# Performance work log

Hardware: AMD Instinct MI355X
Metric: run time of the kernel (lower is better)

Reference implementation:

```python
import jax, jax.numpy as jnp
import numpy as np

B, N, DIM, H, DH = 2, 2048, 1024, 16, 64
INNER = H * DH
EPS = 1e-12  # F.normalize eps
MAX_LOG_SCALE = np.log(1.0 / 0.01)  # clamp max for logit_scale


def setup_inputs() -> dict:
    key = jax.random.key(0)
    k1, k2, k3, k4 = jax.random.split(key, 4)
    x = jax.random.normal(k1, (B, N, DIM), dtype=jnp.float32)
    # Linear weights stored as [in, out] (transpose of torch's [out, in])
    w_qkv = jax.random.normal(k2, (DIM, 3 * INNER), dtype=jnp.float32) * (DIM ** -0.5)
    w_out = jax.random.normal(k3, (INNER, DIM), dtype=jnp.float32) * (INNER ** -0.5)
    b_out = jax.random.normal(k4, (DIM,), dtype=jnp.float32) * 0.01
    logit_scale = jnp.full((H, 1, 1), jnp.log(10.0), dtype=jnp.float32)
    return {"x": x, "w_qkv": w_qkv, "w_out": w_out, "b_out": b_out,
            "logit_scale": logit_scale}


def reference(x, w_qkv, w_out, b_out, logit_scale):
    b, n, dim = x.shape
    h = logit_scale.shape[0]
    qkv = x @ w_qkv                              # [b, n, 3*inner]
    q, k, v = jnp.split(qkv, 3, axis=-1)
    split_heads = lambda t: t.reshape(b, n, h, -1).transpose(0, 2, 1, 3)  # b h n d
    q, k, v = split_heads(q), split_heads(k), split_heads(v)
    # L2-normalize q and k (F.normalize semantics: divide by max(norm, eps))
    qn = q / jnp.maximum(jnp.linalg.norm(q, axis=-1, keepdims=True), EPS)
    kn = k / jnp.maximum(jnp.linalg.norm(k, axis=-1, keepdims=True), EPS)
    scale = jnp.exp(jnp.minimum(logit_scale, MAX_LOG_SCALE))  # [h,1,1], per-head temp
    cos_dots = jnp.einsum('bhid,bhjd->bhij', qn, kn) * scale   # [b,h,n,n]
    # NOTE: masking in the source mutates the unused plain-dot `dots` tensor,
    # so the output never depends on the mask -> faithfully omitted.
    attn = jax.nn.softmax(cos_dots, axis=-1)
    out = jnp.einsum('bhij,bhjd->bhid', attn, v)               # [b,h,n,d]
    out = out.transpose(0, 2, 1, 3).reshape(b, n, -1)          # [b,n,inner]
    return out @ w_out + b_out
```

## Files before the change

### kernel.cpp

```cpp
#include <hip/hip_runtime.h>

typedef __attribute__((ext_vector_type(8))) short bf16x8;
typedef __attribute__((ext_vector_type(4))) float f32x4;
typedef __attribute__((ext_vector_type(16))) float f32x16;
typedef unsigned short u16;
typedef unsigned int u32;
typedef __attribute__((ext_vector_type(4))) unsigned int u32x4;

#define DEV static __device__ __forceinline__

DEV u16 f2bf(float f) {
  u32 u = __float_as_uint(f);
  u += 0x7FFFu + ((u >> 16) & 1u);
  return (u16)(u >> 16);
}
DEV float bf2f(u16 h) { return __uint_as_float(((u32)h) << 16); }

DEV void gload16(const void* g, void* l) {
  __builtin_amdgcn_global_load_lds((const __attribute__((address_space(1))) void*)g,
                                   (__attribute__((address_space(3))) void*)l, 16, 0, 0);
}

#define MFMA16(a, b, c) __builtin_amdgcn_mfma_f32_16x16x32_bf16((a), (b), (c), 0, 0, 0)
#define MFMA32(a, b, c) __builtin_amdgcn_mfma_f32_32x32x16_bf16((a), (b), (c), 0, 0, 0)

DEV u32 cvtpk(float lo, float hi) {
  u32 r;
  asm("v_cvt_pk_bf16_f32 %0, %1, %2" : "=v"(r) : "v"(lo), "v"(hi));
  return r;
}
DEV void plswap(u32& a, u32& b) {
  asm volatile("v_permlane32_swap_b32 %0, %1" : "+v"(a), "+v"(b));
}
DEV bf16x8 asbf(u32x4 v) {
  union { u32x4 u; bf16x8 b; } x;
  x.u = v;
  return x.b;
}

DEV void rawbar() {
  __builtin_amdgcn_sched_barrier(0);
  asm volatile("" ::: "memory");
  __builtin_amdgcn_s_barrier();
  asm volatile("" ::: "memory");
  __builtin_amdgcn_sched_barrier(0);
}
#define VMCNT4() asm volatile("s_waitcnt vmcnt(4)" ::: "memory")
#define VMCNT0() asm volatile("s_waitcnt vmcnt(0)" ::: "memory")
#define LGKM0()  asm volatile("s_waitcnt lgkmcnt(0)" ::: "memory")

#define MAXLOG 4.6051701859880914f

__global__ __launch_bounds__(256) void k_prep(const float* __restrict__ x,
                                              u16* __restrict__ Xbf,
                                              const float* __restrict__ w_qkv,
                                              u16* __restrict__ Wqkvt,
                                              const float* __restrict__ w_out,
                                              u16* __restrict__ Woutt) {
  __shared__ u16 lds[64][72];
  int blk = blockIdx.x;
  int t = threadIdx.x;
  if (blk < 2048) {
    int i = blk * 256 + t;
    const f32x4* p = (const f32x4*)(x + (size_t)i * 8);
    f32x4 a = p[0], b = p[1];
    bf16x8 o;
    o[0] = (short)f2bf(a[0]); o[1] = (short)f2bf(a[1]);
    o[2] = (short)f2bf(a[2]); o[3] = (short)f2bf(a[3]);
    o[4] = (short)f2bf(b[0]); o[5] = (short)f2bf(b[1]);
    o[6] = (short)f2bf(b[2]); o[7] = (short)f2bf(b[3]);
    *(bf16x8*)(Xbf + (size_t)i * 8) = o;
    return;
  }
  const float* src;
  u16* dst;
  int rows, cols, bx, by;
  if (blk < 2816) {
    int q = blk - 2048;
    src = w_qkv; dst = Wqkvt; rows = 1024; cols = 3072;
    bx = q % 48; by = q / 48;
  } else {
    int q = blk - 2816;
    src = w_out; dst = Woutt; rows = 1024; cols = 1024;
    bx = q % 16; by = q / 16;
  }
  int r0 = by * 64, c0 = bx * 64;
  int r = t >> 2, cq = (t & 3) << 4;
  const float* s = src + (size_t)(r0 + r) * cols + c0 + cq;
#pragma unroll
  for (int i = 0; i < 16; i += 4) {
    f32x4 v = *(const f32x4*)(s + i);
    lds[r][cq + i + 0] = f2bf(v[0]);
    lds[r][cq + i + 1] = f2bf(v[1]);
    lds[r][cq + i + 2] = f2bf(v[2]);
    lds[r][cq + i + 3] = f2bf(v[3]);
  }
  __syncthreads();
  int c = t >> 2, rq = (t & 3) << 4;
  bf16x8 o0, o1;
#pragma unroll
  for (int i = 0; i < 8; ++i) o0[i] = (short)lds[rq + i][c];
#pragma unroll
  for (int i = 0; i < 8; ++i) o1[i] = (short)lds[rq + 8 + i][c];
  u16* d = dst + (size_t)(c0 + c) * rows + r0 + rq;
  *(bf16x8*)d = o0;
  *(bf16x8*)(d + 8) = o1;
}

__global__ __launch_bounds__(256) void k_gemm_qkv(const u16* __restrict__ A,
                                                  const u16* __restrict__ Bt,
                                                  const float* __restrict__ logit_scale,
                                                  u16* __restrict__ Qn, u16* __restrict__ Kn,
                                                  u16* __restrict__ Vt,
                                                  int M, int N, int K, int nbx) {
  __shared__ __align__(16) u16 lsA[128 * 64];
  __shared__ __align__(16) u16 lsB[128 * 64];
  int tid = threadIdx.x;
  int lane = tid & 63, wave = tid >> 6;
  int wr = (wave >> 1) * 64, wc = (wave & 1) * 64;
  int nwg = gridDim.x;
  int orig = blockIdx.x;
  int wg = (orig & 7) * (nwg >> 3) + (orig >> 3);
  int bm = (wg / nbx) * 128, bn = (wg % nbx) * 128;

  f32x4 acc[4][4] = {};

  const u16* aSrc[4];
  const u16* bSrc[4];
  int lOf[4];
#pragma unroll
  for (int i = 0; i < 4; ++i) {
    int c = i * 256 + tid;
    int row = c >> 3, ch = c & 7;
    int g = ch ^ (row & 7);
    aSrc[i] = A + (size_t)(bm + row) * K + g * 8;
    bSrc[i] = Bt + (size_t)(bn + row) * K + g * 8;
    lOf[i] = c * 8;
  }

  for (int k0 = 0; k0 < K; k0 += 64) {
    __syncthreads();
#pragma unroll
    for (int i = 0; i < 4; ++i) gload16(aSrc[i] + k0, &lsA[lOf[i]]);
#pragma unroll
    for (int i = 0; i < 4; ++i) gload16(bSrc[i] + k0, &lsB[lOf[i]]);
    __syncthreads();
#pragma unroll
    for (int kk = 0; kk < 2; ++kk) {
      bf16x8 af[4], bfr[4];
#pragma unroll
      for (int m = 0; m < 4; ++m) {
        int r = wr + m * 16 + (lane & 15);
        int p = (kk * 4 + (lane >> 4)) ^ (r & 7);
        af[m] = *(const bf16x8*)&lsA[r * 64 + p * 8];
      }
#pragma unroll
      for (int n = 0; n < 4; ++n) {
        int r = wc + n * 16 + (lane & 15);
        int p = (kk * 4 + (lane >> 4)) ^ (r & 7);
        bfr[n] = *(const bf16x8*)&lsB[r * 64 + p * 8];
      }
#pragma unroll
      for (int m = 0; m < 4; ++m)
#pragma unroll
        for (int n = 0; n < 4; ++n)
          acc[m][n] = MFMA16(af[m], bfr[n], acc[m][n]);
    }
  }

  int colg = bn + wc;
  if (colg < 2048) {
    bool isQ = colg < 1024;
    int h = (colg >> 6) & 15;
    float scale = isQ ? __expf(fminf(logit_scale[h], MAXLOG)) : 1.0f;
    u16* dst = isQ ? Qn : Kn;
#pragma unroll
    for (int m = 0; m < 4; ++m) {
#pragma unroll
      for (int j = 0; j < 4; ++j) {
        float ss = 0.f;
#pragma unroll
        for (int n = 0; n < 4; ++n) ss += acc[m][n][j] * acc[m][n][j];
        ss += __shfl_xor(ss, 1, 64);
        ss += __shfl_xor(ss, 2, 64);
        ss += __shfl_xor(ss, 4, 64);
        ss += __shfl_xor(ss, 8, 64);
        float r = scale / fmaxf(sqrtf(ss), 1e-12f);
        int row = bm + wr + m * 16 + ((lane >> 4) << 2) + j;
        int b = row >> 11, tok = row & 2047;
        size_t base = ((size_t)(b * 16 + h) * 2048 + tok) * 64;
#pragma unroll
        for (int n = 0; n < 4; ++n)
          dst[base + n * 16 + (lane & 15)] = f2bf(acc[m][n][j] * r);
      }
    }
  } else {
    int h = ((colg - 2048) >> 6) & 15;
    __syncthreads();
    u16* sl = (wave < 2 ? lsA : lsB) + (wave & 1) * 2048;
    int bb = bm >> 11, bmm = bm & 2047;
    size_t vbase = ((size_t)(bb * 16 + h) * 64) * 2048;
#pragma unroll
    for (int rr = 0; rr < 2; ++rr) {
#pragma unroll
      for (int nn = 0; nn < 2; ++nn) {
        int n = rr * 2 + nn;
        int d32 = nn * 16 + (lane & 15);
        int xr = (d32 & 7) << 3;
#pragma unroll
        for (int m = 0; m < 4; ++m)
#pragma unroll
          for (int j = 0; j < 4; ++j) {
            int tok = m * 16 + ((lane >> 4) << 2) + j;
            sl[d32 * 64 + (tok ^ xr)] = f2bf(acc[m][n][j]);
          }
      }
      LGKM0();
#pragma unroll
      for (int ri = 0; ri < 4; ++ri) {
        int li = ri * 64 + lane;
        int d32 = li >> 3, c = li & 7;
        int cx = c ^ (d32 & 7);
        bf16x8 v = *(const bf16x8*)&sl[d32 * 64 + cx * 8];
        size_t dsto = vbase + (size_t)(rr * 32 + d32) * 2048 + bmm + wr + c * 8;
        *(bf16x8*)&Vt[dsto] = v;
      }
      LGKM0();
    }
  }
}

__global__ __launch_bounds__(256) void k_gemm_out(const u16* __restrict__ A,
                                                  const u16* __restrict__ Bt,
                                                  float* __restrict__ Cout,
                                                  const float* __restrict__ bias,
                                                  int M, int N, int K, int nbx) {
  __shared__ __align__(16) u16 lsA[128 * 64];
  __shared__ __align__(16) u16 lsB[64 * 64];
  int tid = threadIdx.x;
  int lane = tid & 63, wave = tid >> 6;
  int wr = (wave >> 1) * 64, wc = (wave & 1) * 32;
  int nwg = gridDim.x;
  int orig = blockIdx.x;
  int wg = (orig & 7) * (nwg >> 3) + (orig >> 3);
  int bm = (wg / nbx) * 128, bn = (wg % nbx) * 64;

  f32x4 acc[4][2] = {};

  const u16* aSrc[4];
  const u16* bSrc[2];
  int lOfA[4], lOfB[2];
#pragma unroll
  for (int i = 0; i < 4; ++i) {
    int c = i * 256 + tid;
    int row = c >> 3, ch = c & 7;
    int g = ch ^ (row & 7);
    aSrc[i] = A + (size_t)(bm + row) * K + g * 8;
    lOfA[i] = c * 8;
  }
#pragma unroll
  for (int i = 0; i < 2; ++i) {
    int c = i * 256 + tid;
    int row = c >> 3, ch = c & 7;
    int g = ch ^ (row & 7);
    bSrc[i] = Bt + (size_t)(bn + row) * K + g * 8;
    lOfB[i] = c * 8;
  }

  for (int k0 = 0; k0 < K; k0 += 64) {
    __syncthreads();
#pragma unroll
    for (int i = 0; i < 4; ++i) gload16(aSrc[i] + k0, &lsA[lOfA[i]]);
#pragma unroll
    for (int i = 0; i < 2; ++i) gload16(bSrc[i] + k0, &lsB[lOfB[i]]);
    __syncthreads();
#pragma unroll
    for (int kk = 0; kk < 2; ++kk) {
      bf16x8 af[4], bfr[2];
#pragma unroll
      for (int m = 0; m < 4; ++m) {
        int r = wr + m * 16 + (lane & 15);
        int p = (kk * 4 + (lane >> 4)) ^ (r & 7);
        af[m] = *(const bf16x8*)&lsA[r * 64 + p * 8];
      }
#pragma unroll
      for (int n = 0; n < 2; ++n) {
        int r = wc + n * 16 + (lane & 15);
        int p = (kk * 4 + (lane >> 4)) ^ (r & 7);
        bfr[n] = *(const bf16x8*)&lsB[r * 64 + p * 8];
      }
#pragma unroll
      for (int m = 0; m < 4; ++m)
#pragma unroll
        for (int n = 0; n < 2; ++n)
          acc[m][n] = MFMA16(af[m], bfr[n], acc[m][n]);
    }
  }

#pragma unroll
  for (int m = 0; m < 4; ++m) {
    int row = bm + wr + m * 16 + ((lane >> 4) << 2);
#pragma unroll
    for (int n = 0; n < 2; ++n) {
      int col = bn + wc + n * 16 + (lane & 15);
      float bb = bias[col];
#pragma unroll
      for (int j = 0; j < 4; ++j)
        Cout[(size_t)(row + j) * N + col] = acc[m][n][j] + bb;
    }
  }
}

__global__ __launch_bounds__(256, 2) void k_flash(const u16* __restrict__ Qn,
                                                  const u16* __restrict__ Kn,
                                                  const u16* __restrict__ Vt,
                                                  const float* __restrict__ logit_scale,
                                                  u16* __restrict__ AO) {
  __shared__ __align__(16) u16 lsK[2][64 * 64];
  __shared__ __align__(16) u16 lsV[2][64 * 64];
  __shared__ float l_s[4][32];
  int tid = threadIdx.x, lane = tid & 63, wave = tid >> 6;
  int r31 = lane & 31, h = lane >> 5;
  int bh = blockIdx.x, b = bh >> 4, hd = bh & 15;
  int qw = blockIdx.y * 128 + wave * 32;
  const u16* Q = Qn + (size_t)bh * 2048 * 64;
  const u16* Kb = Kn + (size_t)bh * 2048 * 64;
  const u16* Vb = Vt + (size_t)bh * 64 * 2048;

  float negC = -__expf(fminf(logit_scale[hd], MAXLOG));

  bf16x8 qB[4];
#pragma unroll
  for (int ks = 0; ks < 4; ++ks)
    qB[ks] = *(const bf16x8*)&Q[(size_t)(qw + r31) * 64 + ks * 16 + h * 8];

  size_t kGO[2], vGO[2];
  int lOff[2];
#pragma unroll
  for (int j = 0; j < 2; ++j) {
    int s = j * 256 + tid;
    int row = s >> 3, ch = s & 7, g = ch ^ (row & 7);
    kGO[j] = (size_t)row * 64 + g * 8;
    vGO[j] = (size_t)row * 2048 + g * 8;
    lOff[j] = s * 8;
  }

  int off[2][4];
#pragma unroll
  for (int a = 0; a < 2; ++a)
#pragma unroll
    for (int ks = 0; ks < 4; ++ks)
      off[a][ks] = (a * 32 + r31) * 64 + ((((ks << 1) | h) ^ (r31 & 7)) << 3);

  f32x16 o0, o1;
#pragma unroll
  for (int i = 0; i < 16; ++i) { o0[i] = 0.f; o1[i] = 0.f; }
  float lsm[4] = {0.f, 0.f, 0.f, 0.f};

#define STAGE(dstbuf, kvt)                                          \
  {                                                                 \
    size_t kv0 = (size_t)(kvt) * 64;                                \
    gload16(Kb + kv0 * 64 + kGO[0], &lsK[dstbuf][lOff[0]]);         \
    gload16(Kb + kv0 * 64 + kGO[1], &lsK[dstbuf][lOff[1]]);         \
    gload16(Vb + kv0 + vGO[0], &lsV[dstbuf][lOff[0]]);              \
    gload16(Vb + kv0 + vGO[1], &lsV[dstbuf][lOff[1]]);              \
  }

  STAGE(0, 0);

#pragma unroll 1
  for (int t = 0; t < 32; ++t) {
    int cur = t & 1;
    if (t < 31) {
      STAGE(cur ^ 1, t + 1);
      VMCNT4();
    } else {
      VMCNT0();
    }
    rawbar();
    const u16* Kl = lsK[cur];
    const u16* Vl = lsV[cur];

    f32x16 s0, s1;
#pragma unroll
    for (int i = 0; i < 16; ++i) { s0[i] = negC; s1[i] = negC; }
    bf16x8 k0f[4], k1f[4];
#pragma unroll
    for (int ks = 0; ks < 4; ++ks) {
      k0f[ks] = *(const bf16x8*)&Kl[off[0][ks]];
      k1f[ks] = *(const bf16x8*)&Kl[off[1][ks]];
    }
    __builtin_amdgcn_s_setprio(1);
#pragma unroll
    for (int ks = 0; ks < 4; ++ks) {
      s0 = MFMA32(k0f[ks], qB[ks], s0);
      s1 = MFMA32(k1f[ks], qB[ks], s1);
    }
    __builtin_amdgcn_s_setprio(0);

    bf16x8 v0f[4], v1f[4];
#pragma unroll
    for (int ks = 0; ks < 4; ++ks) {
      v0f[ks] = *(const bf16x8*)&Vl[off[0][ks]];
      v1f[ks] = *(const bf16x8*)&Vl[off[1][ks]];
    }

#pragma unroll
    for (int i = 0; i < 16; ++i) {
      float e0 = __expf(s0[i]);
      float e1 = __expf(s1[i]);
      lsm[i & 3] += e0 + e1;
      s0[i] = e0; s1[i] = e1;
    }

    bf16x8 pa[4];
    {
      u32 c0 = cvtpk(s0[0], s0[1]),  c1 = cvtpk(s0[2], s0[3]);
      u32 c2 = cvtpk(s0[4], s0[5]),  c3 = cvtpk(s0[6], s0[7]);
      u32 c4 = cvtpk(s0[8], s0[9]),  c5 = cvtpk(s0[10], s0[11]);
      u32 c6 = cvtpk(s0[12], s0[13]), c7 = cvtpk(s0[14], s0[15]);
      plswap(c0, c2); plswap(c1, c3); plswap(c4, c6); plswap(c5, c7);
      pa[0] = asbf((u32x4){c0, c1, c2, c3});
      pa[1] = asbf((u32x4){c4, c5, c6, c7});
      u32 d0 = cvtpk(s1[0], s1[1]),  d1 = cvtpk(s1[2], s1[3]);
      u32 d2 = cvtpk(s1[4], s1[5]),  d3 = cvtpk(s1[6], s1[7]);
      u32 d4 = cvtpk(s1[8], s1[9]),  d5 = cvtpk(s1[10], s1[11]);
      u32 d6 = cvtpk(s1[12], s1[13]), d7 = cvtpk(s1[14], s1[15]);
      plswap(d0, d2); plswap(d1, d3); plswap(d4, d6); plswap(d5, d7);
      pa[2] = asbf((u32x4){d0, d1, d2, d3});
      pa[3] = asbf((u32x4){d4, d5, d6, d7});
    }

    __builtin_amdgcn_s_setprio(1);
#pragma unroll
    for (int ks = 0; ks < 4; ++ks) {
      o0 = MFMA32(pa[ks], v0f[ks], o0);
      o1 = MFMA32(pa[ks], v1f[ks], o1);
    }
    __builtin_amdgcn_s_setprio(0);

    rawbar();
  }
#undef STAGE

  float lsum = (lsm[0] + lsm[1]) + (lsm[2] + lsm[3]);
  float ltot = lsum + __shfl_xor(lsum, 32, 64);
  if (h == 0) l_s[wave][r31] = 1.0f / ltot;
  __syncthreads();

#pragma unroll
  for (int r = 0; r < 16; ++r) {
    int cr = (r & 3) + ((r >> 2) << 3) + (h << 2);
    int qr = qw + cr;
    float li = l_s[wave][cr];
    size_t base = ((size_t)(b * 2048 + qr)) * 1024 + hd * 64;
    AO[base + r31] = f2bf(o0[r] * li);
    AO[base + 32 + r31] = f2bf(o1[r] * li);
  }
}

extern "C" void kernel_launch(void* const* d_in, const int* in_sizes, int n_in,
                              void* d_out, int out_size, void* d_ws, size_t ws_size,
                              hipStream_t stream) {
  const float* x = (const float*)d_in[0];
  const float* w_qkv = (const float*)d_in[1];
  const float* w_out = (const float*)d_in[2];
  const float* b_out = (const float*)d_in[3];
  const float* logit_scale = (const float*)d_in[4];

  char* ws = (char*)d_ws;
  u16* Xbf   = (u16*)(ws);
  u16* Wqkvt = (u16*)(ws + (8ll << 20));
  u16* Woutt = (u16*)(ws + (14ll << 20));
  u16* Qn    = (u16*)(ws + (16ll << 20));
  u16* Kn    = (u16*)(ws + (24ll << 20));
  u16* Vt    = (u16*)(ws + (32ll << 20));
  u16* AO    = Xbf;
  float* out = (float*)d_out;

  k_prep<<<3072, 256, 0, stream>>>(x, Xbf, w_qkv, Wqkvt, w_out, Woutt);
  k_gemm_qkv<<<768, 256, 0, stream>>>(Xbf, Wqkvt, logit_scale, Qn, Kn, Vt,
                                      4096, 3072, 1024, 24);
  k_flash<<<dim3(32, 16), 256, 0, stream>>>(Qn, Kn, Vt, logit_scale, AO);
  k_gemm_out<<<512, 256, 0, stream>>>(AO, Woutt, out, b_out,
                                      4096, 1024, 1024, 16);
}
```

Measured before the change: 109.7 us.

## Process two KV tiles per flash iteration with four-buffer LDS pipeline

The flash attention loop now handles two 64-key tiles per iteration. It stages both tiles into a four-deep LDS ring (2 tiles in flight ahead), which halves the number of barriers. Both QK^T products are issued before the exp/PV stages, so the MFMA work of one tile can overlap the softmax of the other. In exchange LDS doubles to 64KB per block and register pressure rises, which may hurt the 2-block occupancy target.

```diff
diff --git a/kernel.cpp b/kernel.cpp
--- a/kernel.cpp
+++ b/kernel.cpp
@@ -45,7 +45,7 @@
   asm volatile("" ::: "memory");
   __builtin_amdgcn_sched_barrier(0);
 }
-#define VMCNT4() asm volatile("s_waitcnt vmcnt(4)" ::: "memory")
+#define VMCNT8() asm volatile("s_waitcnt vmcnt(8)" ::: "memory")
 #define VMCNT0() asm volatile("s_waitcnt vmcnt(0)" ::: "memory")
 #define LGKM0()  asm volatile("s_waitcnt lgkmcnt(0)" ::: "memory")
 
@@ -316,8 +316,8 @@
                                                   const u16* __restrict__ Vt,
                                                   const float* __restrict__ logit_scale,
                                                   u16* __restrict__ AO) {
-  __shared__ __align__(16) u16 lsK[2][64 * 64];
-  __shared__ __align__(16) u16 lsV[2][64 * 64];
+  __shared__ __align__(16) u16 lsK[4][64 * 64];
+  __shared__ __align__(16) u16 lsV[4][64 * 64];
   __shared__ float l_s[4][32];
   int tid = threadIdx.x, lane = tid & 63, wave = tid >> 6;
   int r31 = lane & 31, h = lane >> 5;
@@ -355,7 +355,7 @@
   f32x16 o0, o1;
 #pragma unroll
   for (int i = 0; i < 16; ++i) { o0[i] = 0.f; o1[i] = 0.f; }
-  float lsm[4] = {0.f, 0.f, 0.f, 0.f};
+  float lsm[8] = {0.f, 0.f, 0.f, 0.f, 0.f, 0.f, 0.f, 0.f};
 
 #define STAGE(dstbuf, kvt)                                          \
   {                                                                 \
@@ -366,84 +366,94 @@
     gload16(Vb + kv0 + vGO[1], &lsV[dstbuf][lOff[1]]);              \
   }
 
+#define QKT(S0, S1, BUF)                                            \
+  {                                                                 \
+    bf16x8 k0f[4], k1f[4];                                          \
+    _Pragma("unroll") for (int ks = 0; ks < 4; ++ks) {              \
+      k0f[ks] = *(const bf16x8*)&lsK[BUF][off[0][ks]];              \
+      k1f[ks] = *(const bf16x8*)&lsK[BUF][off[1][ks]];              \
+    }                                                               \
+    _Pragma("unroll") for (int i = 0; i < 16; ++i) { S0[i] = negC; S1[i] = negC; } \
+    __builtin_amdgcn_s_setprio(1);                                  \
+    _Pragma("unroll") for (int ks = 0; ks < 4; ++ks) {              \
+      S0 = MFMA32(k0f[ks], qB[ks], S0);                             \
+      S1 = MFMA32(k1f[ks], qB[ks], S1);                             \
+    }                                                               \
+    __builtin_amdgcn_s_setprio(0);                                  \
+  }
+
+#define EXPT(S0, S1, LB)                                            \
+  _Pragma("unroll") for (int i = 0; i < 16; ++i) {                  \
+    float e0 = __expf(S0[i]);                                       \
+    float e1 = __expf(S1[i]);                                       \
+    lsm[(LB) + (i & 3)] += e0 + e1;                                 \
+    S0[i] = e0; S1[i] = e1;                                         \
+  }
+
+#define PVT(S0, S1, BUF)                                            \
+  {                                                                 \
+    bf16x8 v0f[4], v1f[4];                                          \
+    _Pragma("unroll") for (int ks = 0; ks < 4; ++ks) {              \
+      v0f[ks] = *(const bf16x8*)&lsV[BUF][off[0][ks]];              \
+      v1f[ks] = *(const bf16x8*)&lsV[BUF][off[1][ks]];              \
+    }                                                               \
+    bf16x8 pa[4];                                                   \
+    {                                                               \
+      u32 c0 = cvtpk(S0[0], S0[1]),  c1 = cvtpk(S0[2], S0[3]);      \
+      u32 c2 = cvtpk(S0[4], S0[5]),  c3 = cvtpk(S0[6], S0[7]);      \
+      u32 c4 = cvtpk(S0[8], S0[9]),  c5 = cvtpk(S0[10], S0[11]);    \
+      u32 c6 = cvtpk(S0[12], S0[13]), c7 = cvtpk(S0[14], S0[15]);   \
+      plswap(c0, c2); plswap(c1, c3); plswap(c4, c6); plswap(c5, c7);\
+      pa[0] = asbf((u32x4){c0, c1, c2, c3});                        \
+      pa[1] = asbf((u32x4){c4, c5, c6, c7});                        \
+      u32 d0 = cvtpk(S1[0], S1[1]),  d1 = cvtpk(S1[2], S1[3]);      \
+      u32 d2 = cvtpk(S1[4], S1[5]),  d3 = cvtpk(S1[6], S1[7]);      \
+      u32 d4 = cvtpk(S1[8], S1[9]),  d5 = cvtpk(S1[10], S1[11]);    \
+      u32 d6 = cvtpk(S1[12], S1[13]), d7 = cvtpk(S1[14], S1[15]);   \
+      plswap(d0, d2); plswap(d1, d3); plswap(d4, d6); plswap(d5, d7);\
+      pa[2] = asbf((u32x4){d0, d1, d2, d3});                        \
+      pa[3] = asbf((u32x4){d4, d5, d6, d7});                        \
+    }                                                               \
+    __builtin_amdgcn_s_setprio(1);                                  \
+    _Pragma("unroll") for (int ks = 0; ks < 4; ++ks) {              \
+      o0 = MFMA32(pa[ks], v0f[ks], o0);                             \
+      o1 = MFMA32(pa[ks], v1f[ks], o1);                             \
+    }                                                               \
+    __builtin_amdgcn_s_setprio(0);                                  \
+  }
+
   STAGE(0, 0);
+  STAGE(1, 1);
 
 #pragma unroll 1
-  for (int t = 0; t < 32; ++t) {
-    int cur = t & 1;
-    if (t < 31) {
-      STAGE(cur ^ 1, t + 1);
-      VMCNT4();
+  for (int p = 0; p < 16; ++p) {
+    int cur = (p & 1) << 1;
+    if (p < 15) {
+      STAGE(cur ^ 2, 2 * p + 2);
+      STAGE((cur ^ 2) + 1, 2 * p + 3);
+      VMCNT8();
     } else {
       VMCNT0();
     }
     rawbar();
-    const u16* Kl = lsK[cur];
-    const u16* Vl = lsV[cur];
-
-    f32x16 s0, s1;
-#pragma unroll
-    for (int i = 0; i < 16; ++i) { s0[i] = negC; s1[i] = negC; }
-    bf16x8 k0f[4], k1f[4];
-#pragma unroll
-    for (int ks = 0; ks < 4; ++ks) {
-      k0f[ks] = *(const bf16x8*)&Kl[off[0][ks]];
-      k1f[ks] = *(const bf16x8*)&Kl[off[1][ks]];
-    }
-    __builtin_amdgcn_s_setprio(1);
-#pragma unroll
-    for (int ks = 0; ks < 4; ++ks) {
-      s0 = MFMA32(k0f[ks], qB[ks], s0);
-      s1 = MFMA32(k1f[ks], qB[ks], s1);
-    }
-    __builtin_amdgcn_s_setprio(0);
-
-    bf16x8 v0f[4], v1f[4];
-#pragma unroll
-    for (int ks = 0; ks < 4; ++ks) {
-      v0f[ks] = *(const bf16x8*)&Vl[off[0][ks]];
-      v1f[ks] = *(const bf16x8*)&Vl[off[1][ks]];
-    }
-
-#pragma unroll
-    for (int i = 0; i < 16; ++i) {
-      float e0 = __expf(s0[i]);
-      float e1 = __expf(s1[i]);
-      lsm[i & 3] += e0 + e1;
-      s0[i] = e0; s1[i] = e1;
-    }
-
-    bf16x8 pa[4];
-    {
-      u32 c0 = cvtpk(s0[0], s0[1]),  c1 = cvtpk(s0[2], s0[3]);
-      u32 c2 = cvtpk(s0[4], s0[5]),  c3 = cvtpk(s0[6], s0[7]);
-      u32 c4 = cvtpk(s0[8], s0[9]),  c5 = cvtpk(s0[10], s0[11]);
-      u32 c6 = cvtpk(s0[12], s0[13]), c7 = cvtpk(s0[14], s0[15]);
-      plswap(c0, c2); plswap(c1, c3); plswap(c4, c6); plswap(c5, c7);
-      pa[0] = asbf((u32x4){c0, c1, c2, c3});
-      pa[1] = asbf((u32x4){c4, c5, c6, c7});
-      u32 d0 = cvtpk(s1[0], s1[1]),  d1 = cvtpk(s1[2], s1[3]);
-      u32 d2 = cvtpk(s1[4], s1[5]),  d3 = cvtpk(s1[6], s1[7]);
-      u32 d4 = cvtpk(s1[8], s1[9]),  d5 = cvtpk(s1[10], s1[11]);
-      u32 d6 = cvtpk(s1[12], s1[13]), d7 = cvtpk(s1[14], s1[15]);
-      plswap(d0, d2); plswap(d1, d3); plswap(d4, d6); plswap(d5, d7);
-      pa[2] = asbf((u32x4){d0, d1, d2, d3});
-      pa[3] = asbf((u32x4){d4, d5, d6, d7});
-    }
-
-    __builtin_amdgcn_s_setprio(1);
-#pragma unroll
-    for (int ks = 0; ks < 4; ++ks) {
-      o0 = MFMA32(pa[ks], v0f[ks], o0);
-      o1 = MFMA32(pa[ks], v1f[ks], o1);
-    }
-    __builtin_amdgcn_s_setprio(0);
+
+    f32x16 sA0, sA1, sB0, sB1;
+    QKT(sA0, sA1, cur);
+    QKT(sB0, sB1, cur + 1);
+    EXPT(sA0, sA1, 0);
+    PVT(sA0, sA1, cur);
+    EXPT(sB0, sB1, 4);
+    PVT(sB0, sB1, cur + 1);
 
     rawbar();
   }
 #undef STAGE
-
-  float lsum = (lsm[0] + lsm[1]) + (lsm[2] + lsm[3]);
+#undef QKT
+#undef EXPT
+#undef PVT
+
+  float lsum = ((lsm[0] + lsm[1]) + (lsm[2] + lsm[3])) +
+               ((lsm[4] + lsm[5]) + (lsm[6] + lsm[7]));
   float ltot = lsum + __shfl_xor(lsum, 32, 64);
   if (h == 0) l_s[wave][r31] = 1.0f / ltot;
   __syncthreads();
```

Result: slower. 112.8 us (+2.8%).
